# Kernel tuning notes

Hardware: AMD Instinct MI355X
Metric: run time of the kernel (lower is better)

Reference implementation:

```python
import jax, jax.numpy as jnp
import numpy as np

S = 128          # spatial grid size per axis
N = 100000       # active voxels
C_IN = 32
C_OUT = 32
FS = 3           # filter size per axis -> 27 offsets


def _build_rulebook():
    """Build submanifold-conv rulebook: for each active site and each of the
    27 filter offsets, the index of the active neighbor (or masked out)."""
    rng = np.random.default_rng(0)
    coords = rng.integers(0, S, size=(2 * N, 3))
    lin = coords[:, 0] * S * S + coords[:, 1] * S + coords[:, 2]
    lin = np.unique(lin)[:N]                      # sorted unique active sites
    xyz = np.stack([lin // (S * S), (lin // S) % S, lin % S], axis=1)  # [N,3]
    offs = np.stack(np.meshgrid(*([np.arange(FS) - FS // 2] * 3), indexing='ij'), -1).reshape(-1, 3)  # [27,3]
    nb = xyz[:, None, :] + offs[None, :, :]       # [N,27,3]
    inb = np.all((nb >= 0) & (nb < S), axis=-1)   # in-bounds
    nb_lin = nb[..., 0] * S * S + nb[..., 1] * S + nb[..., 2]
    pos = np.searchsorted(lin, nb_lin)
    pos_c = np.clip(pos, 0, N - 1)
    found = inb & (lin[pos_c] == nb_lin)
    nbr_idx = np.where(found, pos_c, 0).astype(np.int32)   # [N,27]
    return nbr_idx, found


def setup_inputs() -> dict:
    key = jax.random.key(0)
    k1, k2 = jax.random.split(key)
    nbr_idx, nbr_mask = _build_rulebook()
    K = FS ** 3
    std = (2.0 / C_IN / K) ** 0.5   # matches module init
    return {
        'features': jax.random.normal(k1, (N, C_IN), dtype=jnp.float32),
        'weight': std * jax.random.normal(k2, (K, C_IN, C_OUT), dtype=jnp.float32),
        'bias': jnp.zeros((C_OUT,), dtype=jnp.float32),
        'nbr_idx': jnp.asarray(nbr_idx),
        'nbr_mask': jnp.asarray(nbr_mask),
    }


def reference(features, weight, bias, nbr_idx, nbr_mask):
    # Submanifold sparse conv: gather active neighbors per filter offset,
    # multiply by per-offset [Cin,Cout] weight, accumulate at active sites.
    gathered = jnp.where(nbr_mask[:, :, None], features[nbr_idx], 0.0)  # [N,K,Cin]
    out = jnp.einsum('nki,kio->no', gathered, weight) + bias            # [N,Cout]
    return out
```

## Files before the change

kernel.cpp:

```cpp
#include <hip/hip_runtime.h>
#include <hip/hip_bf16.h>

#define NVOX 100000
#define CIN 32
#define COUT 32
#define KOFF 27
#define NTILE 6250

typedef __attribute__((ext_vector_type(8))) short short8;
typedef __attribute__((ext_vector_type(4))) float float4v;

__device__ __forceinline__ short f2bf(float x) {
    union { float f; unsigned u; } v; v.f = x;
    unsigned u = v.u;
    u += 0x7FFFu + ((u >> 16) & 1u);
    return (short)(u >> 16);
}

#define FEAT_BLOCKS 3126

__global__ __launch_bounds__(256) void cvt_kernel(
    const float* __restrict__ feat, const float* __restrict__ weight,
    unsigned short* __restrict__ fbf, short8* __restrict__ wfrag)
{
    if (blockIdx.x < FEAT_BLOCKS) {
        int i = (blockIdx.x * 256 + threadIdx.x) * 4;
        if (i < NVOX * CIN) {
            float4v f = *(const float4v*)(feat + i);
            short s[4] = { f2bf(f.x), f2bf(f.y), f2bf(f.z), f2bf(f.w) };
            *(ulonglong1*)(fbf + i) = *(ulonglong1*)s;
        } else if (i < (NVOX + 1) * CIN) {
            short s[4] = { 0, 0, 0, 0 };
            *(ulonglong1*)(fbf + i) = *(ulonglong1*)s;
        }
    } else {
        int g = (blockIdx.x - FEAT_BLOCKS) * 256 + threadIdx.x;
        if (g >= KOFF * 2 * 64) return;
        int k   = g >> 7;
        int rem = g & 127;
        int t   = rem >> 6;
        int ln  = rem & 63;
        int co  = t * 16 + (ln & 15);
        int cib = (ln >> 4) * 8;
        const float* wp = weight + (k * CIN + cib) * COUT + co;
        short8 b;
#pragma unroll
        for (int j = 0; j < 8; ++j) b[j] = f2bf(wp[j * COUT]);
        wfrag[g] = b;
    }
}

__global__ __launch_bounds__(512, 4) void subm_conv_kernel(
    const unsigned short* __restrict__ fbf,
    const short8* __restrict__ wfrag,
    const float* __restrict__ bias,
    const int* __restrict__ nbr_idx,
    const int* __restrict__ nbr_mask,
    float* __restrict__ out)
{
    __shared__ short8 wlds[KOFF * 2 * 64];

    const int tid  = threadIdx.x;
    const int lane = tid & 63;
    const int wave = tid >> 6;
    const int m    = lane & 15;
    const int quad = lane >> 4;
    const int tile = blockIdx.x * 8 + wave;
    const bool tv  = tile < NTILE;

    const int v0 = tile * 16;
    int v = v0 + m;
    if (v > NVOX - 1) v = NVOX - 1;
    const int base = v * KOFF;

    int enc[KOFF];
#pragma unroll
    for (int k = 0; k < KOFF; ++k) enc[k] = nbr_idx[base + k];
    int mok[KOFF];
#pragma unroll
    for (int k = 0; k < KOFF; ++k) mok[k] = nbr_mask[base + k];
#pragma unroll
    for (int k = 0; k < KOFF; ++k) enc[k] = (mok[k] ? enc[k] : NVOX) << 6;

    for (int g = tid; g < KOFF * 2 * 64; g += 512) wlds[g] = wfrag[g];
    __syncthreads();

    float4v acc0 = {0.f, 0.f, 0.f, 0.f};
    float4v acc1 = {0.f, 0.f, 0.f, 0.f};

    const char* fb   = (const char*)fbf;
    const int   boff = quad * 16;

    short8 abuf[8];
#pragma unroll
    for (int k = 0; k < 8; ++k)
        abuf[k] = *(const short8*)(fb + (size_t)(unsigned)enc[k] + boff);

#pragma unroll
    for (int k = 0; k < KOFF; ++k) {
        const int slot = k & 7;
        short8 a = abuf[slot];
        if (k + 8 < KOFF)
            abuf[slot] = *(const short8*)(fb + (size_t)(unsigned)enc[k + 8] + boff);

        short8 wb0 = wlds[k * 128 + lane];
        short8 wb1 = wlds[k * 128 + 64 + lane];
        acc0 = __builtin_amdgcn_mfma_f32_16x16x32_bf16(a, wb0, acc0, 0, 0, 0);
        acc1 = __builtin_amdgcn_mfma_f32_16x16x32_bf16(a, wb1, acc1, 0, 0, 0);
    }

    __syncthreads();
    float* tb = (float*)wlds + wave * (16 * 36);

    const float bs0 = bias[m];
    const float bs1 = bias[16 + m];
    if (tv) {
#pragma unroll
        for (int r = 0; r < 4; ++r) {
            tb[(quad * 4 + r) * 36 + m]      = acc0[r] + bs0;
            tb[(quad * 4 + r) * 36 + 16 + m] = acc1[r] + bs1;
        }
#pragma unroll
        for (int p = 0; p < 2; ++p) {
            int flat = p * 64 + lane;
            int row  = flat >> 3;
            int ch   = flat & 7;
            float4v val = *(const float4v*)(tb + row * 36 + ch * 4);
            *(float4v*)(out + (size_t)(v0 + row) * COUT + ch * 4) = val;
        }
    }
}

extern "C" void kernel_launch(void* const* d_in, const int* in_sizes, int n_in,
                              void* d_out, int out_size, void* d_ws, size_t ws_size,
                              hipStream_t stream) {
    const float* feat = (const float*)d_in[0];
    const float* wgt  = (const float*)d_in[1];
    const float* bias = (const float*)d_in[2];
    const int*   nidx = (const int*)d_in[3];
    const int*   nmsk = (const int*)d_in[4];
    float*       out  = (float*)d_out;

    char* ws = (char*)d_ws;
    unsigned short* fbf   = (unsigned short*)ws;
    short8*         wfrag = (short8*)(ws + 6400128);

    const int wgt_blocks = (KOFF * 2 * 64 + 255) / 256;
    cvt_kernel<<<FEAT_BLOCKS + wgt_blocks, 256, 0, stream>>>(feat, wgt, fbf, wfrag);

    const int block = 512;
    const int grid  = (NTILE + 7) / 8;
    subm_conv_kernel<<<grid, block, 0, stream>>>(fbf, wfrag, bias, nidx, nmsk, out);
}
```

Before: 99.19 us.

## Coalesce rulebook loads via LDS staging and deepen gather prefetch

Rulebook indices and masks for each 16-voxel tile are now loaded as contiguous int4 vectors across the wave, converted to encoded offsets, staged in shared memory, and then read back per row. This replaces strided per-lane scalar loads. The feature-gather prefetch depth also grows from 8 to 13 offsets to keep more loads in flight. The cost is extra LDS traffic, an added barrier, and higher register pressure that could lower occupancy.

```diff
diff --git a/kernel.cpp b/kernel.cpp
--- a/kernel.cpp
+++ b/kernel.cpp
@@ -6,9 +6,11 @@
 #define COUT 32
 #define KOFF 27
 #define NTILE 6250
+#define KDEPTH 13
 
 typedef __attribute__((ext_vector_type(8))) short short8;
 typedef __attribute__((ext_vector_type(4))) float float4v;
+typedef __attribute__((ext_vector_type(4))) int   int4v;
 
 __device__ __forceinline__ short f2bf(float x) {
     union { float f; unsigned u; } v; v.f = x;
@@ -68,19 +70,41 @@
     const int tile = blockIdx.x * 8 + wave;
     const bool tv  = tile < NTILE;
 
-    const int v0 = tile * 16;
-    int v = v0 + m;
-    if (v > NVOX - 1) v = NVOX - 1;
-    const int base = v * KOFF;
+    const int base4 = tile * 108;
+    const int p4a = lane, p4b = lane + 64;
+    int4v id0{}, mk0{}, id1{}, mk1{};
+    if (tv) {
+        id0 = ((const int4v*)nbr_idx)[base4 + p4a];
+        mk0 = ((const int4v*)nbr_mask)[base4 + p4a];
+        if (p4b < 108) {
+            id1 = ((const int4v*)nbr_idx)[base4 + p4b];
+            mk1 = ((const int4v*)nbr_mask)[base4 + p4b];
+        }
+    }
+
+    int* strip = (int*)wlds + wave * 432;
+    {
+        int4v e0;
+        e0.x = (mk0.x ? id0.x : NVOX) << 6;
+        e0.y = (mk0.y ? id0.y : NVOX) << 6;
+        e0.z = (mk0.z ? id0.z : NVOX) << 6;
+        e0.w = (mk0.w ? id0.w : NVOX) << 6;
+        ((int4v*)strip)[p4a] = e0;
+        if (p4b < 108) {
+            int4v e1;
+            e1.x = (mk1.x ? id1.x : NVOX) << 6;
+            e1.y = (mk1.y ? id1.y : NVOX) << 6;
+            e1.z = (mk1.z ? id1.z : NVOX) << 6;
+            e1.w = (mk1.w ? id1.w : NVOX) << 6;
+            ((int4v*)strip)[p4b] = e1;
+        }
+    }
+    __syncthreads();
 
     int enc[KOFF];
 #pragma unroll
-    for (int k = 0; k < KOFF; ++k) enc[k] = nbr_idx[base + k];
-    int mok[KOFF];
-#pragma unroll
-    for (int k = 0; k < KOFF; ++k) mok[k] = nbr_mask[base + k];
-#pragma unroll
-    for (int k = 0; k < KOFF; ++k) enc[k] = (mok[k] ? enc[k] : NVOX) << 6;
+    for (int k = 0; k < KOFF; ++k) enc[k] = strip[m * KOFF + k];
+    __syncthreads();
 
     for (int g = tid; g < KOFF * 2 * 64; g += 512) wlds[g] = wfrag[g];
     __syncthreads();
@@ -90,18 +114,22 @@
 
     const char* fb   = (const char*)fbf;
     const int   boff = quad * 16;
+    if (!tv) {
+#pragma unroll
+        for (int k = 0; k < KOFF; ++k) enc[k] = NVOX << 6;
+    }
 
-    short8 abuf[8];
+    short8 abuf[KDEPTH];
 #pragma unroll
-    for (int k = 0; k < 8; ++k)
+    for (int k = 0; k < KDEPTH; ++k)
         abuf[k] = *(const short8*)(fb + (size_t)(unsigned)enc[k] + boff);
 
 #pragma unroll
     for (int k = 0; k < KOFF; ++k) {
-        const int slot = k & 7;
+        const int slot = k % KDEPTH;
         short8 a = abuf[slot];
-        if (k + 8 < KOFF)
-            abuf[slot] = *(const short8*)(fb + (size_t)(unsigned)enc[k + 8] + boff);
+        if (k + KDEPTH < KOFF)
+            abuf[slot] = *(const short8*)(fb + (size_t)(unsigned)enc[k + KDEPTH] + boff);
 
         short8 wb0 = wlds[k * 128 + lane];
         short8 wb1 = wlds[k * 128 + 64 + lane];
@@ -114,6 +142,7 @@
 
     const float bs0 = bias[m];
     const float bs1 = bias[16 + m];
+    const int v0 = tile * 16;
     if (tv) {
 #pragma unroll
         for (int r = 0; r < 4; ++r) {
```

New measurement: 99.99 us. No clear change (+0.8%).

## Process two 16-voxel tiles per wave and shrink gather prefetch depth

Applied to the files above, without the earlier changes.

Each wave now computes two 16-voxel tiles, so every LDS weight fragment read feeds four MFMAs instead of two, and the grid is halved. The gather prefetch ring is cut from 8 to 3 entries per tile to hold register pressure down with two tiles in flight. The cost is roughly doubled index/mask registers (54 ints each) per lane and fewer blocks launched (391 instead of 782), which can lower occupancy and latency hiding for the random feature gathers.

```diff
diff --git a/kernel.cpp b/kernel.cpp
--- a/kernel.cpp
+++ b/kernel.cpp
@@ -6,6 +6,7 @@
 #define COUT 32
 #define KOFF 27
 #define NTILE 6250
+#define KDEPTH 3
 
 typedef __attribute__((ext_vector_type(8))) short short8;
 typedef __attribute__((ext_vector_type(4))) float float4v;
@@ -65,68 +66,106 @@
     const int wave = tid >> 6;
     const int m    = lane & 15;
     const int quad = lane >> 4;
-    const int tile = blockIdx.x * 8 + wave;
-    const bool tv  = tile < NTILE;
 
-    const int v0 = tile * 16;
-    int v = v0 + m;
-    if (v > NVOX - 1) v = NVOX - 1;
-    const int base = v * KOFF;
+    const int tA = (blockIdx.x * 8 + wave) * 2;
+    const int tB = tA + 1;
+    const bool tvA = tA < NTILE;
+    const bool tvB = tB < NTILE;
 
-    int enc[KOFF];
+    int vA = tA * 16 + m; if (vA > NVOX - 1) vA = NVOX - 1;
+    int vB = tB * 16 + m; if (vB > NVOX - 1) vB = NVOX - 1;
+    const int baseA = vA * KOFF;
+    const int baseB = vB * KOFF;
+
+    int encA[KOFF], encB[KOFF];
 #pragma unroll
-    for (int k = 0; k < KOFF; ++k) enc[k] = nbr_idx[base + k];
-    int mok[KOFF];
+    for (int k = 0; k < KOFF; ++k) encA[k] = nbr_idx[baseA + k];
 #pragma unroll
-    for (int k = 0; k < KOFF; ++k) mok[k] = nbr_mask[base + k];
+    for (int k = 0; k < KOFF; ++k) encB[k] = nbr_idx[baseB + k];
+    int mokA[KOFF], mokB[KOFF];
 #pragma unroll
-    for (int k = 0; k < KOFF; ++k) enc[k] = (mok[k] ? enc[k] : NVOX) << 6;
+    for (int k = 0; k < KOFF; ++k) mokA[k] = nbr_mask[baseA + k];
+#pragma unroll
+    for (int k = 0; k < KOFF; ++k) mokB[k] = nbr_mask[baseB + k];
+#pragma unroll
+    for (int k = 0; k < KOFF; ++k) encA[k] = (mokA[k] ? encA[k] : NVOX) << 6;
+#pragma unroll
+    for (int k = 0; k < KOFF; ++k) encB[k] = (mokB[k] ? encB[k] : NVOX) << 6;
 
     for (int g = tid; g < KOFF * 2 * 64; g += 512) wlds[g] = wfrag[g];
     __syncthreads();
 
-    float4v acc0 = {0.f, 0.f, 0.f, 0.f};
-    float4v acc1 = {0.f, 0.f, 0.f, 0.f};
+    float4v accA0 = {0.f, 0.f, 0.f, 0.f};
+    float4v accA1 = {0.f, 0.f, 0.f, 0.f};
+    float4v accB0 = {0.f, 0.f, 0.f, 0.f};
+    float4v accB1 = {0.f, 0.f, 0.f, 0.f};
 
     const char* fb   = (const char*)fbf;
     const int   boff = quad * 16;
 
-    short8 abuf[8];
+    short8 abufA[KDEPTH], abufB[KDEPTH];
 #pragma unroll
-    for (int k = 0; k < 8; ++k)
-        abuf[k] = *(const short8*)(fb + (size_t)(unsigned)enc[k] + boff);
+    for (int k = 0; k < KDEPTH; ++k) {
+        abufA[k] = *(const short8*)(fb + (size_t)(unsigned)encA[k] + boff);
+        abufB[k] = *(const short8*)(fb + (size_t)(unsigned)encB[k] + boff);
+    }
 
 #pragma unroll
     for (int k = 0; k < KOFF; ++k) {
-        const int slot = k & 7;
-        short8 a = abuf[slot];
-        if (k + 8 < KOFF)
-            abuf[slot] = *(const short8*)(fb + (size_t)(unsigned)enc[k + 8] + boff);
+        const int slot = k % KDEPTH;
+        short8 aA = abufA[slot];
+        short8 aB = abufB[slot];
+        if (k + KDEPTH < KOFF) {
+            abufA[slot] = *(const short8*)(fb + (size_t)(unsigned)encA[k + KDEPTH] + boff);
+            abufB[slot] = *(const short8*)(fb + (size_t)(unsigned)encB[k + KDEPTH] + boff);
+        }
 
         short8 wb0 = wlds[k * 128 + lane];
         short8 wb1 = wlds[k * 128 + 64 + lane];
-        acc0 = __builtin_amdgcn_mfma_f32_16x16x32_bf16(a, wb0, acc0, 0, 0, 0);
-        acc1 = __builtin_amdgcn_mfma_f32_16x16x32_bf16(a, wb1, acc1, 0, 0, 0);
+        accA0 = __builtin_amdgcn_mfma_f32_16x16x32_bf16(aA, wb0, accA0, 0, 0, 0);
+        accA1 = __builtin_amdgcn_mfma_f32_16x16x32_bf16(aA, wb1, accA1, 0, 0, 0);
+        accB0 = __builtin_amdgcn_mfma_f32_16x16x32_bf16(aB, wb0, accB0, 0, 0, 0);
+        accB1 = __builtin_amdgcn_mfma_f32_16x16x32_bf16(aB, wb1, accB1, 0, 0, 0);
     }
 
     __syncthreads();
-    float* tb = (float*)wlds + wave * (16 * 36);
+    float* tbA = (float*)wlds + wave * 1152;
+    float* tbB = tbA + 576;
 
     const float bs0 = bias[m];
     const float bs1 = bias[16 + m];
-    if (tv) {
+    if (tvA) {
 #pragma unroll
         for (int r = 0; r < 4; ++r) {
-            tb[(quad * 4 + r) * 36 + m]      = acc0[r] + bs0;
-            tb[(quad * 4 + r) * 36 + 16 + m] = acc1[r] + bs1;
+            tbA[(quad * 4 + r) * 36 + m]      = accA0[r] + bs0;
+            tbA[(quad * 4 + r) * 36 + 16 + m] = accA1[r] + bs1;
         }
+    }
+    if (tvB) {
+#pragma unroll
+        for (int r = 0; r < 4; ++r) {
+            tbB[(quad * 4 + r) * 36 + m]      = accB0[r] + bs0;
+            tbB[(quad * 4 + r) * 36 + 16 + m] = accB1[r] + bs1;
+        }
+    }
+    if (tvA) {
 #pragma unroll
         for (int p = 0; p < 2; ++p) {
             int flat = p * 64 + lane;
             int row  = flat >> 3;
             int ch   = flat & 7;
-            float4v val = *(const float4v*)(tb + row * 36 + ch * 4);
-            *(float4v*)(out + (size_t)(v0 + row) * COUT + ch * 4) = val;
+            float4v val = *(const float4v*)(tbA + row * 36 + ch * 4);
+            *(float4v*)(out + (size_t)(tA * 16 + row) * COUT + ch * 4) = val;
+        }
+    }
+    if (tvB) {
+#pragma unroll
+        for (int p = 0; p < 2; ++p) {
+            int flat = p * 64 + lane;
+            int row  = flat >> 3;
+            int ch   = flat & 7;
+            float4v val = *(const float4v*)(tbB + row * 36 + ch * 4);
+            *(float4v*)(out + (size_t)(tB * 16 + row) * COUT + ch * 4) = val;
         }
     }
 }
@@ -149,6 +188,6 @@
     cvt_kernel<<<FEAT_BLOCKS + wgt_blocks, 256, 0, stream>>>(feat, wgt, fbf, wfrag);
 
     const int block = 512;
-    const int grid  = (NTILE + 7) / 8;
+    const int grid  = (NTILE + 15) / 16;
     subm_conv_kernel<<<grid, block, 0, stream>>>(fbf, wfrag, bias, nidx, nmsk, out);
 }
```

Result: slower. 111.8 us (+12.7%).

## Switch to 32x32x16 MFMA tiles with 32-voxel waves and shallower prefetch

Applied to the files above, without the earlier changes.

Each wave now processes 32 voxels using the 32x32x16 bf16 MFMA, splitting Cin into two K-halves. The weight fragment layout in the convert kernel is rebuilt to match. Blocks shrink to 256 threads with waves_per_eu fixed at 2, and the gather prefetch depth drops from 8 offsets to 3. The aim is fewer MFMA issues and better reuse of each gathered row. The trade-offs are lower occupancy and a shallower prefetch, which leaves less latency hiding for the irregular neighbour gathers.

```diff
diff --git a/kernel.cpp b/kernel.cpp
--- a/kernel.cpp
+++ b/kernel.cpp
@@ -5,10 +5,12 @@
 #define CIN 32
 #define COUT 32
 #define KOFF 27
-#define NTILE 6250
+#define NT32 3125
+#define KD 3
 
-typedef __attribute__((ext_vector_type(8))) short short8;
-typedef __attribute__((ext_vector_type(4))) float float4v;
+typedef __attribute__((ext_vector_type(8)))  short  short8;
+typedef __attribute__((ext_vector_type(4)))  float  float4v;
+typedef __attribute__((ext_vector_type(16))) float  float16v;
 
 __device__ __forceinline__ short f2bf(float x) {
     union { float f; unsigned u; } v; v.f = x;
@@ -38,10 +40,10 @@
         if (g >= KOFF * 2 * 64) return;
         int k   = g >> 7;
         int rem = g & 127;
-        int t   = rem >> 6;
+        int h   = rem >> 6;
         int ln  = rem & 63;
-        int co  = t * 16 + (ln & 15);
-        int cib = (ln >> 4) * 8;
+        int co  = ln & 31;
+        int cib = h * 16 + ((ln >> 5) * 8);
         const float* wp = weight + (k * CIN + cib) * COUT + co;
         short8 b;
 #pragma unroll
@@ -50,7 +52,9 @@
     }
 }
 
-__global__ __launch_bounds__(512, 4) void subm_conv_kernel(
+__global__
+__attribute__((amdgpu_flat_work_group_size(256, 256), amdgpu_waves_per_eu(2, 2)))
+void subm_conv_kernel(
     const unsigned short* __restrict__ fbf,
     const short8* __restrict__ wfrag,
     const float* __restrict__ bias,
@@ -63,70 +67,79 @@
     const int tid  = threadIdx.x;
     const int lane = tid & 63;
     const int wave = tid >> 6;
-    const int m    = lane & 15;
-    const int quad = lane >> 4;
-    const int tile = blockIdx.x * 8 + wave;
-    const bool tv  = tile < NTILE;
+    const int r32  = lane & 31;
+    const int half = lane >> 5;
+    const int tile = blockIdx.x * 4 + wave;
+    const bool tv  = tile < NT32;
 
-    const int v0 = tile * 16;
-    int v = v0 + m;
-    if (v > NVOX - 1) v = NVOX - 1;
+    const int v    = tv ? (tile * 32 + r32) : 0;
     const int base = v * KOFF;
 
     int enc[KOFF];
+    if (tv) {
 #pragma unroll
-    for (int k = 0; k < KOFF; ++k) enc[k] = nbr_idx[base + k];
-    int mok[KOFF];
+        for (int k = 0; k < KOFF; ++k) enc[k] = nbr_idx[base + k];
+        int mok[KOFF];
 #pragma unroll
-    for (int k = 0; k < KOFF; ++k) mok[k] = nbr_mask[base + k];
+        for (int k = 0; k < KOFF; ++k) mok[k] = nbr_mask[base + k];
 #pragma unroll
-    for (int k = 0; k < KOFF; ++k) enc[k] = (mok[k] ? enc[k] : NVOX) << 6;
+        for (int k = 0; k < KOFF; ++k) enc[k] = (mok[k] ? enc[k] : NVOX) << 6;
+    } else {
+#pragma unroll
+        for (int k = 0; k < KOFF; ++k) enc[k] = NVOX << 6;
+    }
 
-    for (int g = tid; g < KOFF * 2 * 64; g += 512) wlds[g] = wfrag[g];
+    for (int g = tid; g < KOFF * 2 * 64; g += 256) wlds[g] = wfrag[g];
     __syncthreads();
 
-    float4v acc0 = {0.f, 0.f, 0.f, 0.f};
-    float4v acc1 = {0.f, 0.f, 0.f, 0.f};
+    float16v acc = {};
 
-    const char* fb   = (const char*)fbf;
-    const int   boff = quad * 16;
+    const char* fb = (const char*)fbf;
+    const int  b0 = half * 16;
+    const int  b1 = 32 + half * 16;
 
-    short8 abuf[8];
+    short8 pa[KD], pb[KD];
 #pragma unroll
-    for (int k = 0; k < 8; ++k)
-        abuf[k] = *(const short8*)(fb + (size_t)(unsigned)enc[k] + boff);
+    for (int k = 0; k < KD; ++k) {
+        const char* p = fb + (size_t)(unsigned)enc[k];
+        pa[k] = *(const short8*)(p + b0);
+        pb[k] = *(const short8*)(p + b1);
+    }
 
 #pragma unroll
     for (int k = 0; k < KOFF; ++k) {
-        const int slot = k & 7;
-        short8 a = abuf[slot];
-        if (k + 8 < KOFF)
-            abuf[slot] = *(const short8*)(fb + (size_t)(unsigned)enc[k + 8] + boff);
+        const int slot = k % KD;
+        short8 a0 = pa[slot];
+        short8 a1 = pb[slot];
+        if (k + KD < KOFF) {
+            const char* p = fb + (size_t)(unsigned)enc[k + KD];
+            pa[slot] = *(const short8*)(p + b0);
+            pb[slot] = *(const short8*)(p + b1);
+        }
 
         short8 wb0 = wlds[k * 128 + lane];
         short8 wb1 = wlds[k * 128 + 64 + lane];
-        acc0 = __builtin_amdgcn_mfma_f32_16x16x32_bf16(a, wb0, acc0, 0, 0, 0);
-        acc1 = __builtin_amdgcn_mfma_f32_16x16x32_bf16(a, wb1, acc1, 0, 0, 0);
+        acc = __builtin_amdgcn_mfma_f32_32x32x16_bf16(a0, wb0, acc, 0, 0, 0);
+        acc = __builtin_amdgcn_mfma_f32_32x32x16_bf16(a1, wb1, acc, 0, 0, 0);
     }
 
     __syncthreads();
-    float* tb = (float*)wlds + wave * (16 * 36);
+    float* tb = (float*)wlds + wave * (32 * 36);
 
-    const float bs0 = bias[m];
-    const float bs1 = bias[16 + m];
+    const float bs = bias[r32];
     if (tv) {
 #pragma unroll
-        for (int r = 0; r < 4; ++r) {
-            tb[(quad * 4 + r) * 36 + m]      = acc0[r] + bs0;
-            tb[(quad * 4 + r) * 36 + 16 + m] = acc1[r] + bs1;
+        for (int r = 0; r < 16; ++r) {
+            int row = (r & 3) + 8 * (r >> 2) + 4 * half;
+            tb[row * 36 + r32] = acc[r] + bs;
         }
 #pragma unroll
-        for (int p = 0; p < 2; ++p) {
+        for (int p = 0; p < 4; ++p) {
             int flat = p * 64 + lane;
             int row  = flat >> 3;
             int ch   = flat & 7;
             float4v val = *(const float4v*)(tb + row * 36 + ch * 4);
-            *(float4v*)(out + (size_t)(v0 + row) * COUT + ch * 4) = val;
+            *(float4v*)(out + (size_t)(tile * 32 + row) * COUT + ch * 4) = val;
         }
     }
 }
@@ -148,7 +161,7 @@
     const int wgt_blocks = (KOFF * 2 * 64 + 255) / 256;
     cvt_kernel<<<FEAT_BLOCKS + wgt_blocks, 256, 0, stream>>>(feat, wgt, fbf, wfrag);
 
-    const int block = 512;
-    const int grid  = (NTILE + 7) / 8;
+    const int block = 256;
+    const int grid  = (NT32 + 3) / 4;
     subm_conv_kernel<<<grid, block, 0, stream>>>(fbf, wfrag, bias, nidx, nmsk, out);
 }
```

After: 108.8 us. 9.7% more time.
